# Optimization experiments

Hardware: AMD Instinct MI355X
Metric: run time of the kernel (lower is better)

Reference implementation:

```python
import jax, jax.numpy as jnp
import numpy as np

SHARDS = 8
VOCAB = 50400
VS = VOCAB // SHARDS  # in_dim_per_shard = 6300
D = 4096
SEQ = 2048
B = 4


def setup_inputs() -> dict:
    key = jax.random.key(0)
    k1, k2, k3 = jax.random.split(key, 3)
    x = jax.random.randint(k1, (B, SEQ), 0, VOCAB, dtype=jnp.int32)
    # Dense kernel, vocab-sharded: [shards, Vs, d_model], init stddev 1/sqrt(n_vocab)
    kernel = jax.random.normal(k2, (SHARDS, VS, D), jnp.float32) * (1.0 / np.sqrt(VOCAB))
    bias = jnp.zeros((D,), jnp.float32)  # flax Dense default bias init
    # fixed positional embeddings (all-gathered across shards -> full [seq, d])
    pos_emb = jax.random.normal(k3, (SEQ, D), jnp.float32) * 0.02
    return {"x": x, "kernel": kernel, "bias": bias, "pos_emb": pos_emb}


def reference(x, kernel, bias, pos_emb):
    # Faithful math of the sharded one-hot matmul + psum:
    #   each shard s computes one_hot(clip(x - s*Vs, 0, Vs-1)) @ W_s + bias,
    #   psum over shards => sum_s W_s[clip(x - s*Vs, 0, Vs-1)] + shards * bias.
    # The one-hot matmul is expressed as a direct gather (identical math, no wasted FLOPs).
    shards, vs, d = kernel.shape
    starts = jnp.arange(shards, dtype=x.dtype) * vs  # [shards]

    def step(acc, shard):
        start, W = shard
        idx = jnp.clip(x - start, 0, vs - 1)  # [B, T], clipped per-shard local index
        return acc + W[idx], None  # gather: [B, T, d]

    acc0 = jnp.zeros(x.shape + (d,), kernel.dtype)
    out, _ = jax.lax.scan(step, acc0, (starts, kernel))
    # psum adds each shard's bias; then add all-gathered positional embeddings
    out = out + shards * bias + pos_emb  # [B, T, d] + [d] + [T, d]
    return out
```

## Files before the change

kernel.cpp:

```cpp
#include <hip/hip_runtime.h>


#define SHARDS 8
#define VS 6300
#define DMODEL 4096
#define SEQ 2048
#define NTOK 8192

__global__ __launch_bounds__(256) void precompute_C_kernel(
    const float* __restrict__ kern, const float* __restrict__ bias,
    float* __restrict__ C) {
    int d = blockIdx.x * 256 + threadIdx.x;
    if (d >= DMODEL) return;
    float lo[SHARDS], hi[SHARDS];
#pragma unroll
    for (int s = 0; s < SHARDS; ++s) {
        lo[s] = kern[((size_t)s * VS) * DMODEL + d];
        hi[s] = kern[((size_t)s * VS + (VS - 1)) * DMODEL + d];
    }
    float b8 = 8.0f * bias[d];
    float suf = 0.0f;
    float sufs[SHARDS + 1];
    sufs[SHARDS] = 0.0f;
#pragma unroll
    for (int s = SHARDS - 1; s >= 0; --s) { suf += lo[s]; sufs[s] = suf; }
    float pref = 0.0f;
#pragma unroll
    for (int s = 0; s < SHARDS; ++s) {
        C[(size_t)s * DMODEL + d] = pref + sufs[s + 1] + b8;
        pref += hi[s];
    }
}

__global__ __launch_bounds__(256) void embed_kernel(
    const int* __restrict__ x, const float* __restrict__ kern,
    const float* __restrict__ pos_emb, const float* __restrict__ C,
    float* __restrict__ out) {
    int i = blockIdx.x;
    int t = i & (SEQ - 1);
    int xv = x[i];
    int s = xv / VS;

    const float4* __restrict__ wrow = (const float4*)(kern + (size_t)xv * DMODEL);
    const float4* __restrict__ prow = (const float4*)(pos_emb + (size_t)t * DMODEL);
    const float4* __restrict__ crow = (const float4*)(C + (size_t)s * DMODEL);
    float4* __restrict__ orow = (float4*)(out + (size_t)i * DMODEL);

    int tid = threadIdx.x;
#pragma unroll
    for (int j = 0; j < 4; ++j) {
        int d4 = tid + j * 256;
        float4 w = wrow[d4];
        float4 p = prow[d4];
        float4 c = crow[d4];
        float4 o;
        o.x = w.x + p.x + c.x;
        o.y = w.y + p.y + c.y;
        o.z = w.z + p.z + c.z;
        o.w = w.w + p.w + c.w;
        orow[d4] = o;
    }
}

extern "C" void kernel_launch(void* const* d_in, const int* in_sizes, int n_in,
                              void* d_out, int out_size, void* d_ws, size_t ws_size,
                              hipStream_t stream) {
    const int*   x       = (const int*)d_in[0];
    const float* kern    = (const float*)d_in[1];
    const float* bias    = (const float*)d_in[2];
    const float* pos_emb = (const float*)d_in[3];
    float*       out     = (float*)d_out;
    float*       C       = (float*)d_ws;

    precompute_C_kernel<<<(DMODEL + 255) / 256, 256, 0, stream>>>(kern, bias, C);
    embed_kernel<<<NTOK, 256, 0, stream>>>(x, kern, pos_emb, C, out);
}
```

Baseline: 68.28 us.

## Process four batch tokens per block sharing pos_emb row with software pipelining

Each block now handles the same sequence position across all four batch elements, so it loads the positional-embedding row once and reuses it for four outputs. Loads for the next token are issued before the current one is finished, double-buffering them in registers. Kernel-row loads and output stores use nontemporal hints. The grid shrinks to a quarter and register use per thread rises, which lowers the number of waves available to hide memory latency.

```diff
diff --git a/kernel.cpp b/kernel.cpp
--- a/kernel.cpp
+++ b/kernel.cpp
@@ -6,6 +6,9 @@
 #define DMODEL 4096
 #define SEQ 2048
 #define NTOK 8192
+#define NBLK 2048
+
+typedef float f4 __attribute__((ext_vector_type(4)));
 
 __global__ __launch_bounds__(256) void precompute_C_kernel(
     const float* __restrict__ kern, const float* __restrict__ bias,
@@ -36,30 +39,57 @@
     const int* __restrict__ x, const float* __restrict__ kern,
     const float* __restrict__ pos_emb, const float* __restrict__ C,
     float* __restrict__ out) {
-    int i = blockIdx.x;
-    int t = i & (SEQ - 1);
-    int xv = x[i];
-    int s = xv / VS;
+    const int b   = blockIdx.x;
+    const int tid = threadIdx.x;
 
-    const float4* __restrict__ wrow = (const float4*)(kern + (size_t)xv * DMODEL);
-    const float4* __restrict__ prow = (const float4*)(pos_emb + (size_t)t * DMODEL);
-    const float4* __restrict__ crow = (const float4*)(C + (size_t)s * DMODEL);
-    float4* __restrict__ orow = (float4*)(out + (size_t)i * DMODEL);
+    const int xv0 = x[b];
+    const int xv1 = x[b + NBLK];
+    const int xv2 = x[b + 2 * NBLK];
+    const int xv3 = x[b + 3 * NBLK];
+    const int s0 = xv0 / VS, s1 = xv1 / VS, s2 = xv2 / VS, s3 = xv3 / VS;
 
-    int tid = threadIdx.x;
+    const f4* __restrict__ w0 = (const f4*)(kern + (size_t)xv0 * DMODEL);
+    const f4* __restrict__ w1 = (const f4*)(kern + (size_t)xv1 * DMODEL);
+    const f4* __restrict__ w2 = (const f4*)(kern + (size_t)xv2 * DMODEL);
+    const f4* __restrict__ w3 = (const f4*)(kern + (size_t)xv3 * DMODEL);
+    const f4* __restrict__ c0 = (const f4*)(C + (size_t)s0 * DMODEL);
+    const f4* __restrict__ c1 = (const f4*)(C + (size_t)s1 * DMODEL);
+    const f4* __restrict__ c2 = (const f4*)(C + (size_t)s2 * DMODEL);
+    const f4* __restrict__ c3 = (const f4*)(C + (size_t)s3 * DMODEL);
+    const f4* __restrict__ pr = (const f4*)(pos_emb + (size_t)b * DMODEL);
+
+    f4 p[4];
 #pragma unroll
-    for (int j = 0; j < 4; ++j) {
-        int d4 = tid + j * 256;
-        float4 w = wrow[d4];
-        float4 p = prow[d4];
-        float4 c = crow[d4];
-        float4 o;
-        o.x = w.x + p.x + c.x;
-        o.y = w.y + p.y + c.y;
-        o.z = w.z + p.z + c.z;
-        o.w = w.w + p.w + c.w;
-        orow[d4] = o;
+    for (int j = 0; j < 4; ++j) p[j] = pr[tid + j * 256];
+
+    f4 wA[4], cA[4], wB[4], cB[4];
+
+#define ISSUE(WROW, CROW, W, Cc)                                      \
+    _Pragma("unroll") for (int j = 0; j < 4; ++j)                     \
+        W[j] = __builtin_nontemporal_load(&WROW[tid + j * 256]);      \
+    _Pragma("unroll") for (int j = 0; j < 4; ++j)                     \
+        Cc[j] = CROW[tid + j * 256];
+
+#define FINISH(K, W, Cc)                                              \
+    {                                                                 \
+        f4* __restrict__ orow = (f4*)(out + (size_t)(b + (K) * NBLK) * DMODEL); \
+        _Pragma("unroll") for (int j = 0; j < 4; ++j) {               \
+            f4 o = W[j] + p[j] + Cc[j];                               \
+            __builtin_nontemporal_store(o, &orow[tid + j * 256]);     \
+        }                                                             \
     }
+
+    ISSUE(w0, c0, wA, cA)
+    ISSUE(w1, c1, wB, cB)
+    FINISH(0, wA, cA)
+    ISSUE(w2, c2, wA, cA)
+    FINISH(1, wB, cB)
+    ISSUE(w3, c3, wB, cB)
+    FINISH(2, wA, cA)
+    FINISH(3, wB, cB)
+
+#undef ISSUE
+#undef FINISH
 }
 
 extern "C" void kernel_launch(void* const* d_in, const int* in_sizes, int n_in,
@@ -73,5 +103,5 @@
     float*       C       = (float*)d_ws;
 
     precompute_C_kernel<<<(DMODEL + 255) / 256, 256, 0, stream>>>(kern, bias, C);
-    embed_kernel<<<NTOK, 256, 0, stream>>>(x, kern, pos_emb, C, out);
+    embed_kernel<<<NBLK, 256, 0, stream>>>(x, kern, pos_emb, C, out);
 }
```

Measured after the change: 61.48 us. -9.9%, faster.
